# Performance work log

Hardware: AMD Instinct MI355X
Metric: run time of the kernel (lower is better)

## Reference

```python
import jax, jax.numpy as jnp
import numpy as np


def _dwconv(x, w, b):
    # depthwise conv, NCHW, kernel [C,1,k,k], SAME padding k//2
    k = w.shape[-1]
    p = k // 2
    out = jax.lax.conv_general_dilated(x, w, (1, 1), [(p, p), (p, p)],
                                       feature_group_count=x.shape[1])
    return out + b[None, :, None, None]


def _conv1x1(x, W, b):
    return jnp.einsum('oc,bchw->bohw', W, x) + b[None, :, None, None]


def _ca_weight(q, k):
    # q,k: [b,c,h,w] -> energy [b,h,w,h+w]
    eH = jnp.einsum('bchw,bcgw->bhwg', q, k)  # attend along H (column)
    eW = jnp.einsum('bchw,bchv->bhwv', q, k)  # attend along W (row)
    return jnp.concatenate([eH, eW], axis=3)


def _ca_map(att, v):
    # att: [b,h,w,h+w], v: [b,c,h,w]
    h = v.shape[2]
    outH = jnp.einsum('bcgw,bhwg->bchw', v, att[..., :h])
    outW = jnp.einsum('bchv,bhwv->bchw', v, att[..., h:])
    return outH + outW


def _cc_block(cnn, Wq, bq, Wk, bk, Wv, bv, gamma):
    q = _conv1x1(cnn, Wq, bq)
    k = _conv1x1(cnn, Wk, bk)
    v = _conv1x1(cnn, Wv, bv)
    att = jax.nn.softmax(_ca_weight(q, k), axis=1)  # softmax over H axis, as in torch F.softmax(energy, 1)
    return gamma * _ca_map(att, v) + cnn


def _ppeg(x, w7, b7, w5, b5, w3, b3, H, W):
    C = x.shape[1]
    cnn = x.T.reshape(1, C, H, W)
    out = _dwconv(cnn, w7, b7) + cnn + _dwconv(cnn, w5, b5) + _dwconv(cnn, w3, b3)
    return out.reshape(C, H * W).T  # [N, C]


def setup_inputs() -> dict:
    key = jax.random.key(0)
    N, DIM, HID, QK = 65536, 1024, 512, 64  # N = 256^2
    ks = jax.random.split(key, 26)
    s = 0.02
    inp = {
        'h0': jax.random.normal(ks[0], (N, DIM), jnp.float32),
        'w7': jax.random.normal(ks[1], (DIM, 1, 7, 7)) * s,
        'b7': jax.random.normal(ks[2], (DIM,)) * s,
        'w5': jax.random.normal(ks[3], (DIM, 1, 5, 5)) * s,
        'b5': jax.random.normal(ks[4], (DIM,)) * s,
        'w3': jax.random.normal(ks[5], (DIM, 1, 3, 3)) * s,
        'b3': jax.random.normal(ks[6], (DIM,)) * s,
        'W1': jax.random.normal(ks[7], (HID, DIM)) * s,
        'b1': jax.random.normal(ks[8], (HID,)) * s,
        'Wq': jax.random.normal(ks[9], (QK, HID)) * s,
        'bq': jax.random.normal(ks[10], (QK,)) * s,
        'Wk': jax.random.normal(ks[11], (QK, HID)) * s,
        'bk': jax.random.normal(ks[12], (QK,)) * s,
        'Wv': jax.random.normal(ks[13], (HID, HID)) * s,
        'bv': jax.random.normal(ks[14], (HID,)) * s,
        'gamma': jax.random.normal(ks[15], ()) * 0.5,
        'Wq1': jax.random.normal(ks[16], (QK, HID)) * s,
        'bq1': jax.random.normal(ks[17], (QK,)) * s,
        'Wk1': jax.random.normal(ks[18], (QK, HID)) * s,
        'bk1': jax.random.normal(ks[19], (QK,)) * s,
        'Wv1': jax.random.normal(ks[20], (HID, HID)) * s,
        'bv1': jax.random.normal(ks[21], (HID,)) * s,
        'gamma1': jax.random.normal(ks[22], ()) * 0.5,
        'Wfc': jax.random.normal(ks[23], (1, HID)) * s,
        'bfc': jax.random.normal(ks[24], (1,)) * s,
    }
    return inp


def reference(h0, w7, b7, w5, b5, w3, b3, W1, b1,
              Wq, bq, Wk, bk, Wv, bv, gamma,
              Wq1, bq1, Wk1, bk1, Wv1, bv1, gamma1, Wfc, bfc):
    N = h0.shape[0]
    side = int(np.ceil(np.sqrt(N)))
    pad = side * side - N
    h1 = jnp.concatenate([h0, h0[:pad]], axis=0) if pad > 0 else h0
    # PPEG positional encoding (multi-kernel depthwise conv)
    h1 = _ppeg(h1, w7, b7, w5, b5, w3, b3, side, side)
    # fc1: Linear(1024->512) + ReLU  (h1 already square -> second pad is no-op)
    h2 = jax.nn.relu(h1 @ W1.T + b1)  # [N, 512]
    # CCAttention (two criss-cross blocks + fc to 1 logit)
    cnn = h2.T.reshape(1, h2.shape[1], side, side)
    out = _cc_block(cnn, Wq, bq, Wk, bk, Wv, bv, gamma)
    out1 = _cc_block(out, Wq1, bq1, Wk1, bk1, Wv1, bv1, gamma1)
    out1 = out1.reshape(out1.shape[1], side * side).T  # [N, 512]
    logits = out1 @ Wfc.T + bfc  # [N, 1]
    A = jax.nn.softmax(logits.T, axis=1)  # [1, N] attention over instances
    return A
```

## Files before the change

kernel.cpp:

```cpp
#include <hip/hip_runtime.h>

#define HW 65536
#define SIDE 256

typedef __attribute__((ext_vector_type(8))) short short8v;
typedef __attribute__((ext_vector_type(4))) float f32x4;
typedef __attribute__((ext_vector_type(8))) ushort ushort8v;

__device__ __forceinline__ ushort f2bf(float f) {
  unsigned int u = __builtin_bit_cast(unsigned int, f);
  u = (u + 0x7fff + ((u >> 16) & 1)) >> 16;
  return (ushort)u;
}
__device__ __forceinline__ float bf2f(unsigned int u) {
  return __builtin_bit_cast(float, (u & 0xffffu) << 16);
}
__device__ __forceinline__ float bflo(unsigned int d) {
  return __builtin_bit_cast(float, d << 16);
}
__device__ __forceinline__ float bfhi(unsigned int d) {
  return __builtin_bit_cast(float, d & 0xffff0000u);
}
__device__ __forceinline__ void gld16(const void* g, void* l) {
  __builtin_amdgcn_global_load_lds(
      (const __attribute__((address_space(1))) void*)g,
      (__attribute__((address_space(3))) void*)l, 16, 0, 0);
}

__global__ __launch_bounds__(256) void k_prep(
    const float* __restrict__ W1, const float* __restrict__ Wv,
    const float* __restrict__ Wv1, const float* __restrict__ Wq,
    const float* __restrict__ Wk, const float* __restrict__ Wq1,
    const float* __restrict__ Wk1, const float* __restrict__ bq,
    const float* __restrict__ bk, const float* __restrict__ bq1,
    const float* __restrict__ bk1, const float* __restrict__ w7,
    const float* __restrict__ b7, const float* __restrict__ w5,
    const float* __restrict__ b5, const float* __restrict__ w3,
    const float* __restrict__ b3,
    ushort* __restrict__ W1b, ushort* __restrict__ Wvb,
    ushort* __restrict__ Wv1b, ushort* __restrict__ Wqkb,
    ushort* __restrict__ Wqk1b, float* __restrict__ bqk,
    float* __restrict__ bqk1, float* __restrict__ wc, float* __restrict__ bc) {
  const int i = blockIdx.x * 256 + threadIdx.x;
  if (i < 524288) { W1b[i] = f2bf(W1[i]); return; }
  if (i < 786432) { int j = i - 524288; Wvb[j] = f2bf(Wv[j]); return; }
  if (i < 1048576) { int j = i - 786432; Wv1b[j] = f2bf(Wv1[j]); return; }
  if (i < 1081344) { int j = i - 1048576; Wqkb[j] = f2bf(Wq[j]); return; }
  if (i < 1114112) { int j = i - 1081344; Wqkb[32768 + j] = f2bf(Wk[j]); return; }
  if (i < 1146880) { int j = i - 1114112; Wqk1b[j] = f2bf(Wq1[j]); return; }
  if (i < 1179648) { int j = i - 1146880; Wqk1b[32768 + j] = f2bf(Wk1[j]); return; }
  if (i < 1179904) {
    int j = i - 1179648;
    if (j < 64) bqk[j] = bq[j];
    else if (j < 128) bqk[j] = bk[j - 64];
    else if (j < 192) bqk1[j - 128] = bq1[j - 128];
    else bqk1[j - 128] = bk1[j - 192];
    return;
  }
  if (i < 1180928) {
    const int c = i - 1179904;
    float w[49];
#pragma unroll
    for (int t = 0; t < 49; t++) w[t] = w7[c * 49 + t];
    for (int dy = 0; dy < 5; dy++)
      for (int dx = 0; dx < 5; dx++)
        w[(dy + 1) * 7 + (dx + 1)] += w5[c * 25 + dy * 5 + dx];
    for (int dy = 0; dy < 3; dy++)
      for (int dx = 0; dx < 3; dx++)
        w[(dy + 2) * 7 + (dx + 2)] += w3[c * 9 + dy * 3 + dx];
    w[3 * 7 + 3] += 1.0f;
#pragma unroll
    for (int t = 0; t < 49; t++) wc[c * 49 + t] = w[t];
    bc[c] = b7[c] + b5[c] + b3[c];
  }
}

__global__ __launch_bounds__(256) void k_transpose_nc_v(
    const float* __restrict__ in, ushort* __restrict__ out) {
  __shared__ ushort t[64][64];
  const int c0 = blockIdx.x << 6, r0 = blockIdx.y << 6;
  const int tid = threadIdx.x;
#pragma unroll
  for (int p = 0; p < 2; p++) {
    const int r = (tid >> 3) + p * 32, c8 = tid & 7;
    const float4 f0 = *(const float4*)&in[(size_t)(r0 + r) * 1024 + c0 + c8 * 8];
    const float4 f1 = *(const float4*)&in[(size_t)(r0 + r) * 1024 + c0 + c8 * 8 + 4];
    ushort8v v;
    v[0] = f2bf(f0.x); v[1] = f2bf(f0.y); v[2] = f2bf(f0.z); v[3] = f2bf(f0.w);
    v[4] = f2bf(f1.x); v[5] = f2bf(f1.y); v[6] = f2bf(f1.z); v[7] = f2bf(f1.w);
    *(ushort8v*)&t[r][(c8 ^ ((r >> 3) & 7)) * 8] = v;
  }
  __syncthreads();
#pragma unroll
  for (int p = 0; p < 2; p++) {
    const int c = (tid >> 3) + p * 32, r8 = tid & 7;
    ushort8v v;
#pragma unroll
    for (int j = 0; j < 8; j++) {
      const int rr = r8 * 8 + j;
      v[j] = t[rr][(((c >> 3) ^ r8) << 3) + (c & 7)];
    }
    *(ushort8v*)&out[(size_t)(c0 + c) * HW + r0 + r8 * 8] = v;
  }
}

__global__ __launch_bounds__(256) void k_trv(const ushort* __restrict__ in,
    ushort* __restrict__ out, int R, int C, long long bs) {
  __shared__ ushort t[64][64];
  const size_t base = (size_t)blockIdx.z * bs;
  const int c0 = blockIdx.x << 6, r0 = blockIdx.y << 6;
  const int tid = threadIdx.x;
#pragma unroll
  for (int p = 0; p < 2; p++) {
    const int r = (tid >> 3) + p * 32, c8 = tid & 7;
    const ushort8v v = *(const ushort8v*)&in[base + (size_t)(r0 + r) * C + c0 + c8 * 8];
    *(ushort8v*)&t[r][(c8 ^ ((r >> 3) & 7)) * 8] = v;
  }
  __syncthreads();
#pragma unroll
  for (int p = 0; p < 2; p++) {
    const int c = (tid >> 3) + p * 32, r8 = tid & 7;
    ushort8v v;
#pragma unroll
    for (int j = 0; j < 8; j++) {
      const int rr = r8 * 8 + j;
      v[j] = t[rr][(((c >> 3) ^ r8) << 3) + (c & 7)];
    }
    *(ushort8v*)&out[base + (size_t)(c0 + c) * R + r0 + r8 * 8] = v;
  }
}

__global__ __launch_bounds__(256) void k_dwconv7(const ushort* __restrict__ X,
    const float* __restrict__ wc, const float* __restrict__ bc,
    ushort* __restrict__ out) {
  __shared__ ushort tile[38][272];
  const int c = blockIdx.y;
  const int y0 = blockIdx.x << 5;
  const int tid = threadIdx.x;
  const ushort* Xc = X + (size_t)c * HW;

  float w[49];
#pragma unroll
  for (int i = 0; i < 49; i++) w[i] = wc[c * 49 + i];
  const float bcv = bc[c];

  if (tid < 76) {
    const int r = tid >> 1;
    ushort8v z = {0, 0, 0, 0, 0, 0, 0, 0};
    *(ushort8v*)&tile[r][(tid & 1) ? 264 : 0] = z;
  }
  for (int i = tid; i < 38 * 32; i += 256) {
    const int r = i >> 5, j8 = i & 31;
    const int y = y0 - 3 + r;
    ushort8v v = {0, 0, 0, 0, 0, 0, 0, 0};
    if (y >= 0 && y < SIDE) v = *(const ushort8v*)&Xc[y * SIDE + j8 * 8];
    *(ushort8v*)&tile[r][8 + j8 * 8] = v;
  }
  __syncthreads();

  const int t0 = tid & 63;
  const int ry = (tid >> 6) << 3;
  float acc[8][4] = {};
#pragma unroll
  for (int r = 0; r < 14; r++) {
    const uint2 ua = *(const uint2*)&tile[ry + r][(t0 << 2) + 4];
    const uint2 ub = *(const uint2*)&tile[ry + r][(t0 << 2) + 8];
    const uint2 uc = *(const uint2*)&tile[ry + r][(t0 << 2) + 12];
    float rv[12];
    rv[0] = bflo(ua.x); rv[1] = bfhi(ua.x); rv[2] = bflo(ua.y); rv[3] = bfhi(ua.y);
    rv[4] = bflo(ub.x); rv[5] = bfhi(ub.x); rv[6] = bflo(ub.y); rv[7] = bfhi(ub.y);
    rv[8] = bflo(uc.x); rv[9] = bfhi(uc.x); rv[10] = bflo(uc.y); rv[11] = bfhi(uc.y);
#pragma unroll
    for (int m = 0; m < 8; m++) {
      const int dy = r - m;
      if (dy < 0 || dy > 6) continue;
#pragma unroll
      for (int dx = 0; dx < 7; dx++) {
        const float ww = w[dy * 7 + dx];
#pragma unroll
        for (int o = 0; o < 4; o++) acc[m][o] += ww * rv[o + 1 + dx];
      }
    }
  }
#pragma unroll
  for (int m = 0; m < 8; m++) {
    ushort4 o4 = {f2bf(acc[m][0] + bcv), f2bf(acc[m][1] + bcv),
                  f2bf(acc[m][2] + bcv), f2bf(acc[m][3] + bcv)};
    *(ushort4*)&out[(size_t)c * HW + (y0 + ry + m) * SIDE + (t0 << 2)] = o4;
  }
}

template <int K, int RELU, int TRN>
__global__ __launch_bounds__(512) void k_mm8(
    const ushort* __restrict__ A, int lda,
    const ushort* __restrict__ B, int ldb,
    const float* __restrict__ bias,
    ushort* __restrict__ Cb, int ldc,
    ushort* __restrict__ Ct, int ldt) {
  constexpr int NT = K / 32;
  __shared__ __align__(16) ushort SM[2 * 12288];
  const int tid = threadIdx.x;
  const int lane = tid & 63, wv = tid >> 6;

  const int id = blockIdx.x;
  const int wg = (id & 7) * 128 + (id >> 3);
  const int bm = (wg >> 9) << 8;
  const int bn = (wg & 511) << 7;

  const int l4 = lane >> 2;
  const int sch = (lane & 3) ^ (l4 & 3);
  const int rA0 = (wv * 2) * 16 + l4;
  const int rA1 = (wv * 2 + 1) * 16 + l4;
  const int rB = wv * 16 + l4;
  const ushort* ApS0 = A + (size_t)(bm + rA0) * lda + sch * 8;
  const ushort* ApS1 = A + (size_t)(bm + rA1) * lda + sch * 8;
  const ushort* BpS = B + (size_t)(bn + rB) * ldb + sch * 8;
  const int dA0 = (wv * 2) * 512 + lane * 8;
  const int dA1 = (wv * 2 + 1) * 512 + lane * 8;
  const int dB = wv * 512 + lane * 8;

  const int wm = wv & 3, wn = wv >> 2;
  const int fr = lane & 15, kq = lane >> 4;
  int offA[4], offB[4];
#pragma unroll
  for (int mi = 0; mi < 4; mi++) {
    const int row = wm * 64 + mi * 16 + fr;
    offA[mi] = row * 32 + ((kq ^ (row & 3)) << 3);
  }
#pragma unroll
  for (int ni = 0; ni < 4; ni++) {
    const int row = wn * 64 + ni * 16 + fr;
    offB[ni] = 8192 + row * 32 + ((kq ^ (row & 3)) << 3);
  }

  f32x4 acc[4][4];
#pragma unroll
  for (int mi = 0; mi < 4; mi++)
#pragma unroll
    for (int ni = 0; ni < 4; ni++) acc[mi][ni] = (f32x4){0.f, 0.f, 0.f, 0.f};

#define STAGE8(bufbase, k0)                         \
  do {                                              \
    gld16(ApS0 + (k0), &SM[(bufbase) + dA0]);       \
    gld16(ApS1 + (k0), &SM[(bufbase) + dA1]);       \
    gld16(BpS + (k0), &SM[(bufbase) + 8192 + dB]);  \
  } while (0)

  STAGE8(0, 0);
  STAGE8(12288, 32);
  asm volatile("s_waitcnt vmcnt(3)" ::: "memory");
  __builtin_amdgcn_s_barrier();

  int cur = 0;
#pragma unroll 2
  for (int t = 0; t < NT; ++t) {
    const int base = cur ? 12288 : 0;
    short8v a[4], b2[4];
#pragma unroll
    for (int mi = 0; mi < 4; mi++) a[mi] = *(const short8v*)&SM[base + offA[mi]];
#pragma unroll
    for (int ni = 0; ni < 4; ni++) b2[ni] = *(const short8v*)&SM[base + offB[ni]];
    asm volatile("s_waitcnt lgkmcnt(0)" ::: "memory");
    __builtin_amdgcn_s_barrier();
    const int ts = (t + 2 < NT) ? (t + 2) : (NT - 1);
    STAGE8(base, ts << 5);
    __builtin_amdgcn_s_setprio(1);
#pragma unroll
    for (int mi = 0; mi < 4; mi++)
#pragma unroll
      for (int ni = 0; ni < 4; ni++)
        acc[mi][ni] = __builtin_amdgcn_mfma_f32_16x16x32_bf16(b2[ni], a[mi], acc[mi][ni], 0, 0, 0);
    __builtin_amdgcn_s_setprio(0);
    asm volatile("s_waitcnt vmcnt(3)" ::: "memory");
    __builtin_amdgcn_s_barrier();
    cur ^= 1;
  }
#undef STAGE8
  asm volatile("s_waitcnt vmcnt(0)" ::: "memory");
  __builtin_amdgcn_s_barrier();

  ushort tb[4][4][4];
#pragma unroll
  for (int mi = 0; mi < 4; mi++) {
    const int row = bm + wm * 64 + mi * 16 + fr;
    const float bs1 = bias[row];
#pragma unroll
    for (int ni = 0; ni < 4; ni++) {
      const int col = bn + wn * 64 + ni * 16 + (kq << 2);
      float4 v;
      v.x = acc[mi][ni][0] + bs1; v.y = acc[mi][ni][1] + bs1;
      v.z = acc[mi][ni][2] + bs1; v.w = acc[mi][ni][3] + bs1;
      if (RELU) {
        v.x = fmaxf(v.x, 0.f); v.y = fmaxf(v.y, 0.f);
        v.z = fmaxf(v.z, 0.f); v.w = fmaxf(v.w, 0.f);
      }
      const ushort4 u = {f2bf(v.x), f2bf(v.y), f2bf(v.z), f2bf(v.w)};
      *(ushort4*)&Cb[(size_t)row * ldc + col] = u;
      if (TRN) {
        tb[mi][ni][0] = u.x; tb[mi][ni][1] = u.y;
        tb[mi][ni][2] = u.z; tb[mi][ni][3] = u.w;
      }
    }
  }

  if constexpr (TRN) {
    ushort* St = SM;
#pragma unroll
    for (int hh = 0; hh < 2; hh++) {
      __builtin_amdgcn_s_barrier();
      if (wn == hh) {
#pragma unroll
        for (int mi = 0; mi < 4; mi++) {
          const int cl = wm * 64 + mi * 16 + fr;
#pragma unroll
          for (int ni = 0; ni < 4; ni++) {
            const int nl = ni * 16 + (kq << 2);
#pragma unroll
            for (int r = 0; r < 4; r++) St[(nl + r) * 256 + cl] = tb[mi][ni][r];
          }
        }
      }
      __builtin_amdgcn_s_barrier();
      const int cid = tid * 4;
      const int rowo = cid >> 5;
#pragma unroll
      for (int j = 0; j < 4; j++) {
        const int ch = (cid + j) & 31;
        const ushort8v vv = *(const ushort8v*)&St[rowo * 256 + ch * 8];
        *(ushort8v*)&Ct[(size_t)(bn + hh * 64 + rowo) * ldt + bm + ch * 8] = vv;
      }
    }
  }
}

template <int BN, int BIAS, int RELU, int OUTF, int OUTB, int SWZ>
__global__ __launch_bounds__(256) void k_mm(
    const ushort* __restrict__ A, int lda, long long bsA,
    const ushort* __restrict__ B, int ldb, long long bsB,
    const float* __restrict__ bias,
    float* __restrict__ Cf, ushort* __restrict__ Cb, int ldc, long long bsC,
    int K) {
  static_assert(BN == 64 || BN == 128, "BN");
  constexpr int FN = BN / 32;
  __shared__ __align__(16) ushort SMEM[128 * 32 + BN * 32];
  ushort* As = SMEM;
  ushort* Bs = SMEM + 128 * 32;
  const int tid = threadIdx.x;

  int bx, by, bz;
  if constexpr (SWZ == 0) {
    bx = blockIdx.x; by = blockIdx.y; bz = blockIdx.z;
  } else if constexpr (SWZ == 2) {
    const int id = blockIdx.x, l = id >> 3;
    bz = (id & 7) * 32 + (l >> 2); bx = l & 1; by = (l >> 1) & 1;
  } else {
    const int id = blockIdx.x, l = id >> 3;
    bz = (id & 7) * 32 + (l >> 3); bx = l & 3; by = (l >> 2) & 1;
  }

  const int bm = bx << 7, bn = by * BN;
  const long long zA = (long long)bz * bsA;
  const long long zB = (long long)bz * bsB;
  const long long zC = (long long)bz * bsC;

  const int sr = tid >> 2, sq = tid & 3;
  const int sw0 = (sr >> 1) & 3;
  const int sw1 = ((sr + 64) >> 1) & 3;
  const ushort* Ap0 = A + zA + (size_t)(bm + sr) * lda + ((sq ^ sw0) << 3);
  const ushort* Ap1 = A + zA + (size_t)(bm + sr + 64) * lda + ((sq ^ sw1) << 3);
  const ushort* Bp0 = B + zB + (size_t)(bn + sr) * ldb + ((sq ^ sw0) << 3);
  const ushort* Bp1 = nullptr;
  if constexpr (BN == 128)
    Bp1 = B + zB + (size_t)(bn + sr + 64) * ldb + ((sq ^ sw1) << 3);
  ushort* wA0 = &As[sr * 32 + sq * 8];
  ushort* wA1 = &As[(sr + 64) * 32 + sq * 8];
  ushort* wB0 = &Bs[sr * 32 + sq * 8];
  ushort* wB1 = nullptr;
  if constexpr (BN == 128) wB1 = &Bs[(sr + 64) * 32 + sq * 8];

  const int lane = tid & 63, wv = tid >> 6;
  const int wm = wv & 1, wn = wv >> 1;
  const int fr = lane & 15, kq = lane >> 4;
  int offA[4], offB[FN];
#pragma unroll
  for (int mi = 0; mi < 4; mi++) {
    const int row = wm * 64 + mi * 16 + fr;
    offA[mi] = row * 32 + ((kq ^ ((row >> 1) & 3)) << 3);
  }
#pragma unroll
  for (int ni = 0; ni < FN; ni++) {
    const int row = wn * (BN / 2) + ni * 16 + fr;
    offB[ni] = row * 32 + ((kq ^ ((row >> 1) & 3)) << 3);
  }

  f32x4 acc[4][FN];
#pragma unroll
  for (int mi = 0; mi < 4; mi++)
#pragma unroll
    for (int ni = 0; ni < FN; ni++) acc[mi][ni] = (f32x4){0.f, 0.f, 0.f, 0.f};

  for (int k0 = 0; k0 < K; k0 += 32) {
    __syncthreads();
    gld16(Ap0 + k0, wA0);
    gld16(Ap1 + k0, wA1);
    gld16(Bp0 + k0, wB0);
    if constexpr (BN == 128) gld16(Bp1 + k0, wB1);
    __syncthreads();
    short8v a[4], b[FN];
#pragma unroll
    for (int mi = 0; mi < 4; mi++) a[mi] = *(const short8v*)&As[offA[mi]];
#pragma unroll
    for (int ni = 0; ni < FN; ni++) b[ni] = *(const short8v*)&Bs[offB[ni]];
#pragma unroll
    for (int mi = 0; mi < 4; mi++)
#pragma unroll
      for (int ni = 0; ni < FN; ni++)
        acc[mi][ni] = __builtin_amdgcn_mfma_f32_16x16x32_bf16(b[ni], a[mi], acc[mi][ni], 0, 0, 0);
  }

#pragma unroll
  for (int mi = 0; mi < 4; mi++) {
    const int row = bm + wm * 64 + mi * 16 + fr;
    const float bs1 = (BIAS == 1) ? bias[row] : 0.f;
#pragma unroll
    for (int ni = 0; ni < FN; ni++) {
      const int col = bn + wn * (BN / 2) + ni * 16 + (kq << 2);
      float4 v;
      v.x = acc[mi][ni][0]; v.y = acc[mi][ni][1];
      v.z = acc[mi][ni][2]; v.w = acc[mi][ni][3];
      if (BIAS == 1) { v.x += bs1; v.y += bs1; v.z += bs1; v.w += bs1; }
      if (BIAS == 2) {
        const float4 bc4 = *(const float4*)&bias[col];
        v.x += bc4.x; v.y += bc4.y; v.z += bc4.z; v.w += bc4.w;
      }
      if (RELU) {
        v.x = fmaxf(v.x, 0.f); v.y = fmaxf(v.y, 0.f);
        v.z = fmaxf(v.z, 0.f); v.w = fmaxf(v.w, 0.f);
      }
      const size_t idx = (size_t)(zC + (size_t)row * ldc + col);
      if (OUTF) *(float4*)&Cf[idx] = v;
      if (OUTB) {
        ushort4 u = {f2bf(v.x), f2bf(v.y), f2bf(v.z), f2bf(v.w)};
        *(ushort4*)&Cb[idx] = u;
      }
    }
  }
}

__global__ __launch_bounds__(256) void k_softmax2(const ushort* __restrict__ EW,
    ushort* __restrict__ AW, const ushort* __restrict__ EH,
    ushort* __restrict__ AH) {
  int b = blockIdx.x;
  const ushort* E; ushort* A; int os, hs;
  if (b < 256) { E = EW; A = AW; os = 256; hs = HW; }
  else { E = EH; A = AH; os = HW; hs = 256; b -= 256; }
  const size_t base = (size_t)b * os + threadIdx.x;
  float m = -3.4e38f, s = 0.f;
  for (int h = 0; h < 256; h++) {
    const float x = bf2f(E[base + (size_t)h * hs]);
    const float nm = fmaxf(m, x);
    s = s * __expf(m - nm) + __expf(x - nm);
    m = nm;
  }
  const float inv = 1.0f / s;
  for (int h = 0; h < 256; h++) {
    const size_t i = base + (size_t)h * hs;
    A[i] = f2bf(__expf(bf2f(E[i]) - m) * inv);
  }
}

__global__ __launch_bounds__(256) void k_merge3(const ushort* __restrict__ O,
    const ushort* __restrict__ TH, const ushort* __restrict__ CN,
    const float* __restrict__ gammap, ushort* __restrict__ outB) {
  __shared__ ushort t[64][64];
  const float g = *gammap;
  const size_t base = (size_t)blockIdx.z * HW;
  const int h0 = blockIdx.y << 6, w0 = blockIdx.x << 6;
  const int tid = threadIdx.x;
#pragma unroll
  for (int p = 0; p < 2; p++) {
    const int r = (tid >> 3) + p * 32, c8 = tid & 7;
    const ushort8v v = *(const ushort8v*)&TH[base + (w0 + r) * SIDE + h0 + c8 * 8];
    *(ushort8v*)&t[r][(c8 ^ ((r >> 3) & 7)) * 8] = v;
  }
  __syncthreads();
#pragma unroll
  for (int p = 0; p < 2; p++) {
    const int h = (tid >> 3) + p * 32, r8 = tid & 7;
    const size_t idx = base + (h0 + h) * SIDE + w0 + r8 * 8;
    const ushort8v o8 = *(const ushort8v*)&O[idx];
    const ushort8v c8v = *(const ushort8v*)&CN[idx];
    ushort8v res;
#pragma unroll
    for (int j = 0; j < 8; j++) {
      const int rr = r8 * 8 + j;
      const float th = bf2f(t[rr][(((h >> 3) ^ r8) << 3) + (h & 7)]);
      res[j] = f2bf(g * (bf2f(o8[j]) + th) + bf2f(c8v[j]));
    }
    *(ushort8v*)&outB[idx] = res;
  }
}

__global__ __launch_bounds__(256) void k_logits(const ushort* __restrict__ X,
    const float* __restrict__ Wfc, const float* __restrict__ bfc,
    float* __restrict__ L) {
  const int n = blockIdx.x * 256 + threadIdx.x;
  float s = 0.f;
  for (int j = 0; j < 512; j++) s += bf2f(X[(size_t)j * HW + n]) * Wfc[j];
  L[n] = s + bfc[0];
}

__global__ __launch_bounds__(256) void k_smax_reduce(const float* __restrict__ L,
                                                     float* __restrict__ red) {
  __shared__ float sm[256];
  const int tid = threadIdx.x;
  float m = -3.4e38f;
  for (int i = tid; i < HW; i += 256) m = fmaxf(m, L[i]);
  sm[tid] = m;
  __syncthreads();
  for (int s = 128; s > 0; s >>= 1) {
    if (tid < s) sm[tid] = fmaxf(sm[tid], sm[tid + s]);
    __syncthreads();
  }
  const float M = sm[0];
  __syncthreads();
  float sum = 0.f;
  for (int i = tid; i < HW; i += 256) sum += expf(L[i] - M);
  sm[tid] = sum;
  __syncthreads();
  for (int s = 128; s > 0; s >>= 1) {
    if (tid < s) sm[tid] += sm[tid + s];
    __syncthreads();
  }
  if (tid == 0) { red[0] = M; red[1] = sm[0]; }
}

__global__ __launch_bounds__(256) void k_smax_write(const float* __restrict__ L,
    const float* __restrict__ red, float* __restrict__ out) {
  const int n = blockIdx.x * 256 + threadIdx.x;
  out[n] = expf(L[n] - red[0]) * (1.0f / red[1]);
}

extern "C" void kernel_launch(void* const* d_in, const int* in_sizes, int n_in,
                              void* d_out, int out_size, void* d_ws, size_t ws_size,
                              hipStream_t stream) {
  const float* h0 = (const float*)d_in[0];
  const float* w7 = (const float*)d_in[1];
  const float* b7 = (const float*)d_in[2];
  const float* w5 = (const float*)d_in[3];
  const float* b5 = (const float*)d_in[4];
  const float* w3 = (const float*)d_in[5];
  const float* b3 = (const float*)d_in[6];
  const float* W1 = (const float*)d_in[7];
  const float* b1 = (const float*)d_in[8];
  const float* Wq = (const float*)d_in[9];
  const float* bq = (const float*)d_in[10];
  const float* Wk = (const float*)d_in[11];
  const float* bk = (const float*)d_in[12];
  const float* Wv = (const float*)d_in[13];
  const float* bv = (const float*)d_in[14];
  const float* gamma = (const float*)d_in[15];
  const float* Wq1 = (const float*)d_in[16];
  const float* bq1 = (const float*)d_in[17];
  const float* Wk1 = (const float*)d_in[18];
  const float* bk1 = (const float*)d_in[19];
  const float* Wv1 = (const float*)d_in[20];
  const float* bv1 = (const float*)d_in[21];
  const float* gamma1 = (const float*)d_in[22];
  const float* Wfc = (const float*)d_in[23];
  const float* bfc = (const float*)d_in[24];

  char* W = (char*)d_ws;
  const size_t MB = 1 << 20;
  ushort* Xb    = (ushort*)(W + 0);
  ushort* H2b   = (ushort*)(W + 0);
  ushort* H2t   = (ushort*)(W + 64 * MB);
  ushort* qkt   = (ushort*)(W + 128 * MB);
  ushort* AttW  = (ushort*)(W + 144 * MB);
  ushort* AttH  = (ushort*)(W + 176 * MB);
  ushort* H1b   = (ushort*)(W + 256 * MB);
  ushort* H1t   = (ushort*)(W + 384 * MB);
  ushort* Vb    = (ushort*)(W + 384 * MB);
  ushort* vTb   = (ushort*)(W + 448 * MB);
  ushort* Ob    = (ushort*)(W + 512 * MB);
  ushort* THbb  = (ushort*)(W + 576 * MB);
  ushort* EbW   = (ushort*)(W + 640 * MB);
  ushort* EbH   = (ushort*)(W + 672 * MB);
  ushort* W1b   = (ushort*)(W + 704 * MB);
  ushort* Wvb   = (ushort*)(W + 705 * MB);
  ushort* Wv1b  = (ushort*)(W + 705 * MB + 512 * 1024);
  ushort* Wqkb  = (ushort*)(W + 706 * MB);
  ushort* Wqk1b = (ushort*)(W + 706 * MB + 128 * 1024);
  float*  wcomb = (float*)(W + 706 * MB + 256 * 1024);
  float*  bcomb = (float*)(W + 706 * MB + 464 * 1024);
  float*  bqk   = (float*)(W + 706 * MB + 472 * 1024);
  float*  bqk1  = (float*)(W + 706 * MB + 474 * 1024);
  float*  L     = (float*)(W + 707 * MB);
  float*  red   = (float*)(W + 707 * MB + 256 * 1024);

  k_prep<<<4613, 256, 0, stream>>>(W1, Wv, Wv1, Wq, Wk, Wq1, Wk1,
                                   bq, bk, bq1, bk1, w7, b7, w5, b5, w3, b3,
                                   W1b, Wvb, Wv1b, Wqkb, Wqk1b, bqk, bqk1,
                                   wcomb, bcomb);

  k_transpose_nc_v<<<dim3(16, 1024), 256, 0, stream>>>(h0, Xb);
  k_dwconv7<<<dim3(8, 1024), 256, 0, stream>>>(Xb, wcomb, bcomb, H1b);
  k_trv<<<dim3(1024, 16, 1), 256, 0, stream>>>(H1b, H1t, 1024, HW, 0);

  k_mm8<1024, 1, 1><<<1024, 512, 0, stream>>>(
      W1b, 1024, H1t, 1024, b1, H2b, HW, H2t, 512);

  auto cc_block = [&](const ushort* act, ushort* cnn, const ushort* Wqk_,
                      const float* bqk_, const ushort* Wv_, const float* bv_,
                      const float* gam) {
    k_mm<128, 2, 0, 0, 1, 0><<<dim3(512, 1, 1), 256, 0, stream>>>(
        act, 512, 0, Wqk_, 512, 0, bqk_, nullptr, qkt, 128, 0, 512);
    k_mm8<512, 0, 0><<<1024, 512, 0, stream>>>(
        Wv_, 512, act, 512, bv_, Vb, HW, nullptr, 0);
    k_trv<<<dim3(4, 4, 512), 256, 0, stream>>>(Vb, vTb, 256, 256, 65536);
    k_mm<128, 0, 0, 0, 1, 2><<<1024, 256, 0, stream>>>(
        qkt, 128, 32768, qkt + 64, 128, 32768, nullptr, nullptr, EbW, 256,
        65536, 64);
    k_mm<128, 0, 0, 0, 1, 2><<<1024, 256, 0, stream>>>(
        qkt, 32768, 128, qkt + 64, 32768, 128, nullptr, nullptr, EbH, 256,
        65536, 64);
    k_softmax2<<<512, 256, 0, stream>>>(EbW, AttW, EbH, AttH);
    k_mm<128, 0, 0, 0, 1, 3><<<2048, 256, 0, stream>>>(
        Vb, HW, 256, AttW, 256, 65536, nullptr, nullptr, Ob, HW, 256, 256);
    k_mm<128, 0, 0, 0, 1, 3><<<2048, 256, 0, stream>>>(
        vTb, HW, 256, AttH, 256, 65536, nullptr, nullptr, THbb, HW, 256, 256);
    k_merge3<<<dim3(4, 4, 512), 256, 0, stream>>>(Ob, THbb, cnn, gam, cnn);
  };

  cc_block(H2t, H2b, Wqkb, bqk, Wvb, bv, gamma);
  k_trv<<<dim3(1024, 8, 1), 256, 0, stream>>>(H2b, H2t, 512, HW, 0);
  cc_block(H2t, H2b, Wqk1b, bqk1, Wv1b, bv1, gamma1);

  k_logits<<<256, 256, 0, stream>>>(H2b, Wfc, bfc, L);
  k_smax_reduce<<<1, 256, 0, stream>>>(L, red);
  k_smax_write<<<256, 256, 0, stream>>>(L, red, (float*)d_out);
}
```

Baseline: 1.220 ms.

## Merge paired criss-cross GEMM launches and vectorize softmax and logits loads

The two energy GEMMs (row and column) now run as one launch, and so do the two attention-apply GEMMs. A section index taken from the block id selects which operand set each block uses. The column softmax and the logits kernel now read two bf16 values per 32-bit load and do half as many threads' worth of launches. The aim is to cut launch count and tail idle time between small dependent kernels and to widen memory accesses. In exchange, the A, B and C pointers lose __restrict__, which may limit compiler optimizations in the GEMM.

```diff
diff --git a/kernel.cpp b/kernel.cpp
--- a/kernel.cpp
+++ b/kernel.cpp
@@ -335,11 +335,13 @@
 
 template <int BN, int BIAS, int RELU, int OUTF, int OUTB, int SWZ>
 __global__ __launch_bounds__(256) void k_mm(
-    const ushort* __restrict__ A, int lda, long long bsA,
-    const ushort* __restrict__ B, int ldb, long long bsB,
+    const ushort* A, int lda, long long bsA,
+    const ushort* B, int ldb, long long bsB,
     const float* __restrict__ bias,
-    float* __restrict__ Cf, ushort* __restrict__ Cb, int ldc, long long bsC,
-    int K) {
+    float* __restrict__ Cf, ushort* Cb, int ldc, long long bsC,
+    const ushort* A2, int lda2, long long bsA2,
+    const ushort* B2, int ldb2, long long bsB2,
+    ushort* Cb2, int K) {
   static_assert(BN == 64 || BN == 128, "BN");
   constexpr int FN = BN / 32;
   __shared__ __align__(16) ushort SMEM[128 * 32 + BN * 32];
@@ -347,15 +349,32 @@
   ushort* Bs = SMEM + 128 * 32;
   const int tid = threadIdx.x;
 
-  int bx, by, bz;
+  int bx, by, bz, sec = 0;
   if constexpr (SWZ == 0) {
     bx = blockIdx.x; by = blockIdx.y; bz = blockIdx.z;
   } else if constexpr (SWZ == 2) {
     const int id = blockIdx.x, l = id >> 3;
     bz = (id & 7) * 32 + (l >> 2); bx = l & 1; by = (l >> 1) & 1;
+  } else if constexpr (SWZ == 3) {
+    const int id = blockIdx.x, l = id >> 3;
+    bz = (id & 7) * 32 + (l >> 3); bx = l & 3; by = (l >> 2) & 1;
+  } else if constexpr (SWZ == 4) {
+    const int id = blockIdx.x, l = id >> 3;
+    sec = l >> 7;
+    const int l2 = l & 127;
+    bz = (id & 7) * 32 + (l2 >> 2); bx = l2 & 1; by = (l2 >> 1) & 1;
   } else {
     const int id = blockIdx.x, l = id >> 3;
-    bz = (id & 7) * 32 + (l >> 3); bx = l & 3; by = (l >> 2) & 1;
+    sec = l >> 8;
+    const int l2 = l & 255;
+    bz = (id & 7) * 32 + (l2 >> 3); bx = l2 & 3; by = (l2 >> 2) & 1;
+  }
+  if constexpr (SWZ >= 4) {
+    if (sec) {
+      A = A2; lda = lda2; bsA = bsA2;
+      B = B2; ldb = ldb2; bsB = bsB2;
+      Cb = Cb2;
+    }
   }
 
   const int bm = bx << 7, bn = by * BN;
@@ -447,25 +466,38 @@
   }
 }
 
-__global__ __launch_bounds__(256) void k_softmax2(const ushort* __restrict__ EW,
+__global__ __launch_bounds__(256) void k_softmax2v(const ushort* __restrict__ EW,
     ushort* __restrict__ AW, const ushort* __restrict__ EH,
     ushort* __restrict__ AH) {
-  int b = blockIdx.x;
-  const ushort* E; ushort* A; int os, hs;
-  if (b < 256) { E = EW; A = AW; os = 256; hs = HW; }
-  else { E = EH; A = AH; os = HW; hs = 256; b -= 256; }
-  const size_t base = (size_t)b * os + threadIdx.x;
-  float m = -3.4e38f, s = 0.f;
+  const int b = blockIdx.x, tid = threadIdx.x;
+  const ushort* E;
+  ushort* A;
+  size_t base;
+  int hs;
+  if (b < 128) {
+    E = EW; A = AW; hs = HW;
+    base = (size_t)b * 512 + tid * 2;
+  } else {
+    E = EH; A = AH; hs = 256;
+    const int w = (b - 128) * 2 + (tid >> 7);
+    base = (size_t)w * HW + (tid & 127) * 2;
+  }
+  float m0 = -3.4e38f, m1 = -3.4e38f, s0 = 0.f, s1 = 0.f;
   for (int h = 0; h < 256; h++) {
-    const float x = bf2f(E[base + (size_t)h * hs]);
-    const float nm = fmaxf(m, x);
-    s = s * __expf(m - nm) + __expf(x - nm);
-    m = nm;
-  }
-  const float inv = 1.0f / s;
+    const unsigned int u = *(const unsigned int*)&E[base + (size_t)h * hs];
+    const float x0 = bflo(u), x1 = bfhi(u);
+    const float n0 = fmaxf(m0, x0), n1 = fmaxf(m1, x1);
+    s0 = s0 * __expf(m0 - n0) + __expf(x0 - n0);
+    s1 = s1 * __expf(m1 - n1) + __expf(x1 - n1);
+    m0 = n0; m1 = n1;
+  }
+  const float i0 = 1.0f / s0, i1 = 1.0f / s1;
   for (int h = 0; h < 256; h++) {
-    const size_t i = base + (size_t)h * hs;
-    A[i] = f2bf(__expf(bf2f(E[i]) - m) * inv);
+    const size_t idx = base + (size_t)h * hs;
+    const unsigned int u = *(const unsigned int*)&E[idx];
+    const ushort r0 = f2bf(__expf(bflo(u) - m0) * i0);
+    const ushort r1 = f2bf(__expf(bfhi(u) - m1) * i1);
+    *(unsigned int*)&A[idx] = (unsigned int)r0 | ((unsigned int)r1 << 16);
   }
 }
 
@@ -501,13 +533,19 @@
   }
 }
 
-__global__ __launch_bounds__(256) void k_logits(const ushort* __restrict__ X,
+__global__ __launch_bounds__(256) void k_logits2(const ushort* __restrict__ X,
     const float* __restrict__ Wfc, const float* __restrict__ bfc,
     float* __restrict__ L) {
-  const int n = blockIdx.x * 256 + threadIdx.x;
-  float s = 0.f;
-  for (int j = 0; j < 512; j++) s += bf2f(X[(size_t)j * HW + n]) * Wfc[j];
-  L[n] = s + bfc[0];
+  const int n0 = (blockIdx.x * 256 + threadIdx.x) * 2;
+  float s0 = 0.f, s1 = 0.f;
+  for (int j = 0; j < 512; j++) {
+    const unsigned int u = *(const unsigned int*)&X[(size_t)j * HW + n0];
+    const float wj = Wfc[j];
+    s0 += bflo(u) * wj;
+    s1 += bfhi(u) * wj;
+  }
+  float2 o = {s0 + bfc[0], s1 + bfc[0]};
+  *(float2*)&L[n0] = o;
 }
 
 __global__ __launch_bounds__(256) void k_smax_reduce(const float* __restrict__ L,
@@ -614,21 +652,18 @@
                       const float* bqk_, const ushort* Wv_, const float* bv_,
                       const float* gam) {
     k_mm<128, 2, 0, 0, 1, 0><<<dim3(512, 1, 1), 256, 0, stream>>>(
-        act, 512, 0, Wqk_, 512, 0, bqk_, nullptr, qkt, 128, 0, 512);
+        act, 512, 0, Wqk_, 512, 0, bqk_, nullptr, qkt, 128, 0,
+        nullptr, 0, 0, nullptr, 0, 0, nullptr, 512);
     k_mm8<512, 0, 0><<<1024, 512, 0, stream>>>(
         Wv_, 512, act, 512, bv_, Vb, HW, nullptr, 0);
     k_trv<<<dim3(4, 4, 512), 256, 0, stream>>>(Vb, vTb, 256, 256, 65536);
-    k_mm<128, 0, 0, 0, 1, 2><<<1024, 256, 0, stream>>>(
+    k_mm<128, 0, 0, 0, 1, 4><<<2048, 256, 0, stream>>>(
         qkt, 128, 32768, qkt + 64, 128, 32768, nullptr, nullptr, EbW, 256,
-        65536, 64);
-    k_mm<128, 0, 0, 0, 1, 2><<<1024, 256, 0, stream>>>(
-        qkt, 32768, 128, qkt + 64, 32768, 128, nullptr, nullptr, EbH, 256,
-        65536, 64);
-    k_softmax2<<<512, 256, 0, stream>>>(EbW, AttW, EbH, AttH);
-    k_mm<128, 0, 0, 0, 1, 3><<<2048, 256, 0, stream>>>(
-        Vb, HW, 256, AttW, 256, 65536, nullptr, nullptr, Ob, HW, 256, 256);
-    k_mm<128, 0, 0, 0, 1, 3><<<2048, 256, 0, stream>>>(
-        vTb, HW, 256, AttH, 256, 65536, nullptr, nullptr, THbb, HW, 256, 256);
+        65536, qkt, 32768, 128, qkt + 64, 32768, 128, EbH, 64);
+    k_softmax2v<<<256, 256, 0, stream>>>(EbW, AttW, EbH, AttH);
+    k_mm<128, 0, 0, 0, 1, 5><<<4096, 256, 0, stream>>>(
+        Vb, HW, 256, AttW, 256, 65536, nullptr, nullptr, Ob, HW, 256,
+        vTb, HW, 256, AttH, 256, 65536, THbb, 256);
     k_merge3<<<dim3(4, 4, 512), 256, 0, stream>>>(Ob, THbb, cnn, gam, cnn);
   };
 
@@ -636,7 +671,7 @@
   k_trv<<<dim3(1024, 8, 1), 256, 0, stream>>>(H2b, H2t, 512, HW, 0);
   cc_block(H2t, H2b, Wqk1b, bqk1, Wv1b, bv1, gamma1);
 
-  k_logits<<<256, 256, 0, stream>>>(H2b, Wfc, bfc, L);
+  k_logits2<<<128, 256, 0, stream>>>(H2b, Wfc, bfc, L);
   k_smax_reduce<<<1, 256, 0, stream>>>(L, red);
   k_smax_write<<<256, 256, 0, stream>>>(L, red, (float*)d_out);
 }
```

Result: slower. 1.276 ms (+4.5%).
